# Optimization experiments

Measured on AMD Instinct MI355X. Metric: run time of the kernel, lower is better.

The kernel has to match this reference:

```python
import jax, jax.numpy as jnp
import numpy as np

B, S, D, H = 32, 578, 1024, 16  # seq = (384//16)**2 + 2 = 578
DH = D // H  # 64, per-head size
INIT_STD = 0.02


def setup_inputs() -> dict:
    key = jax.random.key(0)
    ks = jax.random.split(key, 7)
    hidden_states = jax.random.normal(ks[0], (B, S, D), dtype=jnp.float32)
    # Per-head Dense layers: stack H separate [D, DH] kernels -> [H, D, DH]
    Wq = jax.random.normal(ks[1], (H, D, DH), dtype=jnp.float32) * INIT_STD
    Wk = jax.random.normal(ks[2], (H, D, DH), dtype=jnp.float32) * INIT_STD
    Wv = jax.random.normal(ks[3], (H, D, DH), dtype=jnp.float32) * INIT_STD
    bq = jax.random.normal(ks[4], (H, DH), dtype=jnp.float32) * INIT_STD
    bk = jax.random.normal(ks[5], (H, DH), dtype=jnp.float32) * INIT_STD
    bv = jax.random.normal(ks[6], (H, DH), dtype=jnp.float32) * INIT_STD
    return {"hidden_states": hidden_states, "Wq": Wq, "bq": bq,
            "Wk": Wk, "bk": bk, "Wv": Wv, "bv": bv}


def reference(hidden_states, Wq, bq, Wk, bk, Wv, bv):
    # Per-head Dense projections (original: Python list of H Dense layers),
    # expressed as one batched einsum over the head axis.
    # hidden_states: [B, S, D]; W*: [H, D, E]; b*: [H, E]
    q = jnp.einsum('bsd,hde->bhse', hidden_states, Wq) + bq[None, :, None, :]
    k = jnp.einsum('bsd,hde->bhse', hidden_states, Wk) + bk[None, :, None, :]
    v = jnp.einsum('bsd,hde->bhse', hidden_states, Wv) + bv[None, :, None, :]
    scale = 1.0 / jnp.sqrt(jnp.asarray(DH, dtype=q.dtype))
    scores = jnp.einsum('bhse,bhte->bhst', q, k) * scale  # [B, H, S, S]
    probs = jax.nn.softmax(scores, axis=-1)  # stable_softmax; dropout p=0
    out = jnp.einsum('bhst,bhte->bhse', probs, v)  # [B, H, S, E]
    # concat heads along last axis -> [B, S, H*E]
    return out.transpose(0, 2, 1, 3).reshape(B, S, H * DH)
```

## Files before the change

kernel.cpp:

```cpp
#include <hip/hip_runtime.h>

typedef __attribute__((ext_vector_type(8))) short short8;
typedef __attribute__((ext_vector_type(4))) float f32x4;
typedef unsigned short u16;
typedef unsigned int u32;

#define B_ 32
#define S_ 578
#define D_ 1024
#define H_ 16
#define DH_ 64
#define M_ 18496
#define MP_ 18560
#define N_ 3072
#define K_ 1024
#define ST_ 640
#define BHROWS_ (B_ * H_ * S_ + 64)
#define SCALE2 0.18033688011112042f
#define CMAX 16.0f

__device__ __forceinline__ u16 f2bf(float x) {
  u32 u = __float_as_uint(x);
  u = (u + 0x7fffu + ((u >> 16) & 1u)) >> 16;
  return (u16)u;
}

__device__ __forceinline__ void gload_lds16(const u16* g, u16* l) {
  __builtin_amdgcn_global_load_lds((const __attribute__((address_space(1))) void*)g,
                                   (__attribute__((address_space(3))) void*)l, 16, 0, 0);
}

__global__ __launch_bounds__(256) void cvt_hidden(const float* __restrict__ in, u16* __restrict__ o) {
  long i = ((long)blockIdx.x * 256 + threadIdx.x) * 8;
  float4 f0 = *(const float4*)(in + i);
  float4 f1 = *(const float4*)(in + i + 4);
  short8 v;
  u16* p = (u16*)&v;
  p[0] = f2bf(f0.x); p[1] = f2bf(f0.y); p[2] = f2bf(f0.z); p[3] = f2bf(f0.w);
  p[4] = f2bf(f1.x); p[5] = f2bf(f1.y); p[6] = f2bf(f1.z); p[7] = f2bf(f1.w);
  *(short8*)(o + i) = v;
}

__global__ __launch_bounds__(256) void wt_kernel(const float* __restrict__ Wq, const float* __restrict__ Wk,
                                                 const float* __restrict__ Wv, u16* __restrict__ Wt) {
  const int d0 = blockIdx.x * 64;
  const int h = blockIdx.y;
  const int qkv = blockIdx.z;
  const float* W = (qkv == 0) ? Wq : ((qkv == 1) ? Wk : Wv);
  __shared__ float tile[64][65];
  const int t = threadIdx.x;
  {
    int e = t & 63, dr = t >> 6;
#pragma unroll
    for (int p = 0; p < 16; ++p) {
      int dd = dr + p * 4;
      tile[dd][e] = W[((long)h * D_ + d0 + dd) * DH_ + e];
    }
  }
  __syncthreads();
  {
    int dd = t & 63, er = t >> 6;
#pragma unroll
    for (int p = 0; p < 16; ++p) {
      int ee = er + p * 4;
      long n = (long)qkv * 1024 + h * 64 + ee;
      Wt[n * K_ + d0 + dd] = f2bf(tile[dd][ee]);
    }
  }
}

__global__ __launch_bounds__(256) void bias_kernel(const float* __restrict__ bq, const float* __restrict__ bk,
                                                   const float* __restrict__ bv, float* __restrict__ bias) {
  int i = blockIdx.x * 256 + threadIdx.x;
  if (i < 3072) {
    const float* src = (i < 1024) ? bq : ((i < 2048) ? bk : bv);
    bias[i] = src[i & 1023];
  }
}

__global__ __launch_bounds__(256) void qkv_gemm(const u16* __restrict__ A, const u16* __restrict__ Bt,
                                                const float* __restrict__ bias,
                                                u16* __restrict__ qb, u16* __restrict__ kb, u16* __restrict__ vbt) {
  __shared__ alignas(16) u16 As[128 * 32];
  __shared__ alignas(16) u16 Bs[128 * 32];
  const int tid = threadIdx.x, wave = tid >> 6, lane = tid & 63, quad = lane >> 4, l16 = lane & 15;
  const long m0 = (long)blockIdx.x * 128, n0 = (long)blockIdx.y * 128;
  const u16* Ag = A + m0 * K_;
  const u16* Bg = Bt + n0 * K_;

  f32x4 acc[4][4];
#pragma unroll
  for (int mi = 0; mi < 4; ++mi)
#pragma unroll
    for (int ni = 0; ni < 4; ++ni) { f32x4 z = {0.f, 0.f, 0.f, 0.f}; acc[mi][ni] = z; }

  const int srow = lane >> 2;
  const int gchunk = (lane & 3) ^ ((lane >> 3) & 3);
  const int scol = gchunk * 8;
  const int r0 = 32 * wave;
  const int sw = quad ^ ((l16 >> 1) & 3);
  const int rb = (wave >> 1) * 64 + l16;
  const int cb = (wave & 1) * 64 + l16;

  for (int it = 0; it < 32; ++it) {
    const int k0 = it * 32;
    gload_lds16(Ag + (long)(r0 + srow) * K_ + k0 + scol,      &As[r0 * 32 + lane * 8]);
    gload_lds16(Ag + (long)(r0 + 16 + srow) * K_ + k0 + scol, &As[(r0 + 16) * 32 + lane * 8]);
    gload_lds16(Bg + (long)(r0 + srow) * K_ + k0 + scol,      &Bs[r0 * 32 + lane * 8]);
    gload_lds16(Bg + (long)(r0 + 16 + srow) * K_ + k0 + scol, &Bs[(r0 + 16) * 32 + lane * 8]);
    __syncthreads();
    const short8* Asv = (const short8*)As;
    const short8* Bsv = (const short8*)Bs;
    short8 a[4], b2[4];
#pragma unroll
    for (int mi = 0; mi < 4; ++mi) a[mi] = Asv[(rb + mi * 16) * 4 + sw];
#pragma unroll
    for (int ni = 0; ni < 4; ++ni) b2[ni] = Bsv[(cb + ni * 16) * 4 + sw];
#pragma unroll
    for (int mi = 0; mi < 4; ++mi)
#pragma unroll
      for (int ni = 0; ni < 4; ++ni)
        acc[mi][ni] = __builtin_amdgcn_mfma_f32_16x16x32_bf16(a[mi], b2[ni], acc[mi][ni], 0, 0, 0);
    __syncthreads();
  }

  float bv4[4]; int hh[4], ee[4];
#pragma unroll
  for (int ni = 0; ni < 4; ++ni) {
    long n = n0 + (wave & 1) * 64 + ni * 16 + l16;
    bv4[ni] = bias[n];
    hh[ni] = (int)((n >> 6) & 15);
    ee[ni] = (int)(n & 63);
  }
  const int qkv = (int)(n0 >> 10);
  if (qkv == 2) {
#pragma unroll
    for (int mi = 0; mi < 4; ++mi) {
#pragma unroll
      for (int r = 0; r < 4; ++r) {
        long m = m0 + (wave >> 1) * 64 + mi * 16 + quad * 4 + r;
        if (m < M_) {
          unsigned bi = (unsigned)m / (unsigned)S_;
          unsigned si = (unsigned)m - bi * (unsigned)S_;
#pragma unroll
          for (int ni = 0; ni < 4; ++ni) {
            float v = acc[mi][ni][r] + bv4[ni];
            vbt[((long)(bi * H_ + hh[ni]) * DH_ + ee[ni]) * ST_ + si] = f2bf(v);
          }
        }
      }
    }
  } else {
    u16* dst = (qkv == 0) ? qb : kb;
#pragma unroll
    for (int mi = 0; mi < 4; ++mi) {
#pragma unroll
      for (int r = 0; r < 4; ++r) {
        long m = m0 + (wave >> 1) * 64 + mi * 16 + quad * 4 + r;
        if (m < M_) {
          unsigned bi = (unsigned)m / (unsigned)S_;
          unsigned si = (unsigned)m - bi * (unsigned)S_;
          long rowb = ((long)bi * H_) * S_ * DH_ + (long)si * DH_;
#pragma unroll
          for (int ni = 0; ni < 4; ++ni) {
            float v = acc[mi][ni][r] + bv4[ni];
            dst[rowb + (long)hh[ni] * (S_ * DH_) + ee[ni]] = f2bf(v);
          }
        }
      }
    }
  }
}

__global__ __launch_bounds__(256) void attn_kernel(const u16* __restrict__ qb, const u16* __restrict__ kb,
                                                   const u16* __restrict__ vbt, float* __restrict__ out) {
  __shared__ alignas(16) u16 Ks[64 * 64];
  __shared__ alignas(16) u16 Vs[64 * 64];
  __shared__ alignas(16) u16 Ps[4 * 16 * 72];
  const int tid = threadIdx.x, wave = tid >> 6, lane = tid & 63, quad = lane >> 4, l16 = lane & 15;
  const int qt = blockIdx.x, h = blockIdx.y, b = blockIdx.z;
  const long bh = (long)b * H_ + h;
  const u16* qp = qb + bh * S_ * DH_;
  const u16* kp = kb + bh * S_ * DH_;
  const u16* vtp = vbt + bh * DH_ * ST_;
  const int q0 = qt * 64;

  short8 qf0, qf1;
  {
    int row = q0 + wave * 16 + l16;
    const short8* qv = (const short8*)(qp + (long)row * DH_);
    qf0 = qv[quad];
    qf1 = qv[4 + quad];
  }

  f32x4 O[4];
#pragma unroll
  for (int et = 0; et < 4; ++et) { f32x4 z = {0.f, 0.f, 0.f, 0.f}; O[et] = z; }
  float lp[4] = {0.f, 0.f, 0.f, 0.f};

  const int srow0 = tid >> 3;
  const int slot = tid & 7;
  const int s0 = quad ^ (l16 & 7);

  for (int kt = 0; kt < 10; ++kt) {
    const int t0 = kt * 64;
    __syncthreads();
#pragma unroll
    for (int p = 0; p < 2; ++p) {
      int row = srow0 + 32 * p;
      int gch = slot ^ (row & 7);
      gload_lds16(kp + (long)(t0 + row) * DH_ + gch * 8, &Ks[(tid + 256 * p) * 8]);
      gload_lds16(vtp + (long)row * ST_ + t0 + gch * 8, &Vs[(tid + 256 * p) * 8]);
    }
    __syncthreads();

    float p[4][4];
    const short8* Kv8 = (const short8*)Ks;
#pragma unroll
    for (int jt = 0; jt < 4; ++jt) {
      f32x4 sacc = {0.f, 0.f, 0.f, 0.f};
      short8 kf0 = Kv8[(16 * jt + l16) * 8 + s0];
      short8 kf1 = Kv8[(16 * jt + l16) * 8 + ((quad + 4) ^ (l16 & 7))];
      sacc = __builtin_amdgcn_mfma_f32_16x16x32_bf16(qf0, kf0, sacc, 0, 0, 0);
      sacc = __builtin_amdgcn_mfma_f32_16x16x32_bf16(qf1, kf1, sacc, 0, 0, 0);
      bool valid = (t0 + 16 * jt + l16) < S_;
#pragma unroll
      for (int r = 0; r < 4; ++r) {
        float e = valid ? exp2f(sacc[r] * SCALE2 - CMAX) : 0.f;
        p[jt][r] = e;
        lp[r] += e;
      }
    }

    u16* Pw = Ps + wave * 16 * 72;
#pragma unroll
    for (int jt = 0; jt < 4; ++jt)
#pragma unroll
      for (int r = 0; r < 4; ++r)
        Pw[(quad * 4 + r) * 72 + 16 * jt + l16] = f2bf(p[jt][r]);

    const short8* Pv8 = (const short8*)(Ps + wave * 16 * 72);
    const short8* Vv8 = (const short8*)Vs;
#pragma unroll
    for (int ks = 0; ks < 2; ++ks) {
      short8 pa = Pv8[l16 * 9 + ks * 4 + quad];
#pragma unroll
      for (int et = 0; et < 4; ++et) {
        short8 vf = Vv8[(16 * et + l16) * 8 + ((ks * 4 + quad) ^ (l16 & 7))];
        O[et] = __builtin_amdgcn_mfma_f32_16x16x32_bf16(pa, vf, O[et], 0, 0, 0);
      }
    }
  }

  float inv[4];
#pragma unroll
  for (int r = 0; r < 4; ++r) {
    float s = lp[r];
    s += __shfl_xor(s, 1);
    s += __shfl_xor(s, 2);
    s += __shfl_xor(s, 4);
    s += __shfl_xor(s, 8);
    inv[r] = 1.0f / s;
  }
#pragma unroll
  for (int et = 0; et < 4; ++et)
#pragma unroll
    for (int r = 0; r < 4; ++r) {
      int s = q0 + wave * 16 + quad * 4 + r;
      if (s < S_) out[((long)b * S_ + s) * (H_ * DH_) + (long)h * DH_ + et * 16 + l16] = O[et][r] * inv[r];
    }
}

extern "C" void kernel_launch(void* const* d_in, const int* in_sizes, int n_in,
                              void* d_out, int out_size, void* d_ws, size_t ws_size,
                              hipStream_t stream) {
  const float* hs = (const float*)d_in[0];
  const float* Wq = (const float*)d_in[1];
  const float* bq = (const float*)d_in[2];
  const float* Wk = (const float*)d_in[3];
  const float* bk = (const float*)d_in[4];
  const float* Wv = (const float*)d_in[5];
  const float* bv = (const float*)d_in[6];
  float* out = (float*)d_out;

  u16* Abf = (u16*)d_ws;
  u16* Wt = Abf + (size_t)MP_ * K_;
  float* bias = (float*)(Wt + (size_t)N_ * K_);
  u16* qb = (u16*)(bias + N_);
  u16* kb = qb + (size_t)BHROWS_ * DH_;
  u16* vbt = kb + (size_t)BHROWS_ * DH_;

  cvt_hidden<<<dim3(9248), dim3(256), 0, stream>>>(hs, Abf);
  wt_kernel<<<dim3(16, 16, 3), dim3(256), 0, stream>>>(Wq, Wk, Wv, Wt);
  bias_kernel<<<dim3(12), dim3(256), 0, stream>>>(bq, bk, bv, bias);
  qkv_gemm<<<dim3(145, 24), dim3(256), 0, stream>>>(Abf, Wt, bias, qb, kb, vbt);
  attn_kernel<<<dim3(10, 16, 32), dim3(256), 0, stream>>>(qb, kb, vbt, out);
}
```

Measured before the change: 478.8 us.

## Deepen GEMM K-tile, remap GEMM blocks, and double per-wave query rows in attention

The QKV GEMM now loads 64-wide K tiles, which halves the number of barriers. It also uses a 1D grid whose block-index remap groups the N tiles sharing an M tile on neighbouring blocks, to improve L2 reuse of A. The attention kernel handles 128 queries per block (32 per wave), so each K/V tile loaded into LDS serves twice as many rows. S is now computed transposed (K as the A operand), the P stores are packed, and row sums are reduced through LDS. In exchange the kernel uses more registers and LDS, and the launch has fewer attention blocks, which lowers occupancy and parallelism.

```diff
diff --git a/kernel.cpp b/kernel.cpp
--- a/kernel.cpp
+++ b/kernel.cpp
@@ -81,10 +81,14 @@
 __global__ __launch_bounds__(256) void qkv_gemm(const u16* __restrict__ A, const u16* __restrict__ Bt,
                                                 const float* __restrict__ bias,
                                                 u16* __restrict__ qb, u16* __restrict__ kb, u16* __restrict__ vbt) {
-  __shared__ alignas(16) u16 As[128 * 32];
-  __shared__ alignas(16) u16 Bs[128 * 32];
+  __shared__ alignas(16) u16 As[128 * 64];
+  __shared__ alignas(16) u16 Bs[128 * 64];
   const int tid = threadIdx.x, wave = tid >> 6, lane = tid & 63, quad = lane >> 4, l16 = lane & 15;
-  const long m0 = (long)blockIdx.x * 128, n0 = (long)blockIdx.y * 128;
+  const int id = blockIdx.x;
+  const int jj = id >> 3;
+  const int m_t = jj / 3;
+  const int n_t = (id & 7) * 3 + (jj - m_t * 3);
+  const long m0 = (long)m_t * 128, n0 = (long)n_t * 128;
   const u16* Ag = A + m0 * K_;
   const u16* Bg = Bt + n0 * K_;
 
@@ -94,33 +98,36 @@
 #pragma unroll
     for (int ni = 0; ni < 4; ++ni) { f32x4 z = {0.f, 0.f, 0.f, 0.f}; acc[mi][ni] = z; }
 
-  const int srow = lane >> 2;
-  const int gchunk = (lane & 3) ^ ((lane >> 3) & 3);
-  const int scol = gchunk * 8;
-  const int r0 = 32 * wave;
-  const int sw = quad ^ ((l16 >> 1) & 3);
+  const int srow = tid >> 3;
+  const int gch8 = (((tid & 7) ^ ((tid >> 3) & 7))) * 8;
+  const int fsw = l16 & 7;
   const int rb = (wave >> 1) * 64 + l16;
   const int cb = (wave & 1) * 64 + l16;
 
-  for (int it = 0; it < 32; ++it) {
-    const int k0 = it * 32;
-    gload_lds16(Ag + (long)(r0 + srow) * K_ + k0 + scol,      &As[r0 * 32 + lane * 8]);
-    gload_lds16(Ag + (long)(r0 + 16 + srow) * K_ + k0 + scol, &As[(r0 + 16) * 32 + lane * 8]);
-    gload_lds16(Bg + (long)(r0 + srow) * K_ + k0 + scol,      &Bs[r0 * 32 + lane * 8]);
-    gload_lds16(Bg + (long)(r0 + 16 + srow) * K_ + k0 + scol, &Bs[(r0 + 16) * 32 + lane * 8]);
+  for (int it = 0; it < 16; ++it) {
+    const int k0 = it * 64;
+#pragma unroll
+    for (int i = 0; i < 4; ++i) {
+      gload_lds16(Ag + (long)(srow + 32 * i) * K_ + k0 + gch8, &As[(tid + 256 * i) * 8]);
+      gload_lds16(Bg + (long)(srow + 32 * i) * K_ + k0 + gch8, &Bs[(tid + 256 * i) * 8]);
+    }
     __syncthreads();
     const short8* Asv = (const short8*)As;
     const short8* Bsv = (const short8*)Bs;
-    short8 a[4], b2[4];
-#pragma unroll
-    for (int mi = 0; mi < 4; ++mi) a[mi] = Asv[(rb + mi * 16) * 4 + sw];
-#pragma unroll
-    for (int ni = 0; ni < 4; ++ni) b2[ni] = Bsv[(cb + ni * 16) * 4 + sw];
-#pragma unroll
-    for (int mi = 0; mi < 4; ++mi)
-#pragma unroll
-      for (int ni = 0; ni < 4; ++ni)
-        acc[mi][ni] = __builtin_amdgcn_mfma_f32_16x16x32_bf16(a[mi], b2[ni], acc[mi][ni], 0, 0, 0);
+#pragma unroll
+    for (int kk = 0; kk < 2; ++kk) {
+      short8 a[4], b2[4];
+      const int sl = (kk * 4 + quad) ^ fsw;
+#pragma unroll
+      for (int mi = 0; mi < 4; ++mi) a[mi] = Asv[(rb + mi * 16) * 8 + sl];
+#pragma unroll
+      for (int ni = 0; ni < 4; ++ni) b2[ni] = Bsv[(cb + ni * 16) * 8 + sl];
+#pragma unroll
+      for (int mi = 0; mi < 4; ++mi)
+#pragma unroll
+        for (int ni = 0; ni < 4; ++ni)
+          acc[mi][ni] = __builtin_amdgcn_mfma_f32_16x16x32_bf16(a[mi], b2[ni], acc[mi][ni], 0, 0, 0);
+    }
     __syncthreads();
   }
 
@@ -176,98 +183,120 @@
                                                    const u16* __restrict__ vbt, float* __restrict__ out) {
   __shared__ alignas(16) u16 Ks[64 * 64];
   __shared__ alignas(16) u16 Vs[64 * 64];
-  __shared__ alignas(16) u16 Ps[4 * 16 * 72];
+  __shared__ alignas(16) u16 Ps[4][32 * 72];
+  __shared__ float Ls[4][32];
   const int tid = threadIdx.x, wave = tid >> 6, lane = tid & 63, quad = lane >> 4, l16 = lane & 15;
   const int qt = blockIdx.x, h = blockIdx.y, b = blockIdx.z;
   const long bh = (long)b * H_ + h;
   const u16* qp = qb + bh * S_ * DH_;
   const u16* kp = kb + bh * S_ * DH_;
   const u16* vtp = vbt + bh * DH_ * ST_;
-  const int q0 = qt * 64;
-
-  short8 qf0, qf1;
-  {
-    int row = q0 + wave * 16 + l16;
+  const int q0 = qt * 128;
+
+  short8 qf[2][2];
+#pragma unroll
+  for (int g = 0; g < 2; ++g) {
+    int row = q0 + wave * 32 + g * 16 + l16;
     const short8* qv = (const short8*)(qp + (long)row * DH_);
-    qf0 = qv[quad];
-    qf1 = qv[4 + quad];
-  }
-
-  f32x4 O[4];
-#pragma unroll
-  for (int et = 0; et < 4; ++et) { f32x4 z = {0.f, 0.f, 0.f, 0.f}; O[et] = z; }
-  float lp[4] = {0.f, 0.f, 0.f, 0.f};
-
-  const int srow0 = tid >> 3;
-  const int slot = tid & 7;
-  const int s0 = quad ^ (l16 & 7);
+    qf[g][0] = qv[quad];
+    qf[g][1] = qv[4 + quad];
+  }
+
+  f32x4 O[2][4];
+#pragma unroll
+  for (int g = 0; g < 2; ++g)
+#pragma unroll
+    for (int et = 0; et < 4; ++et) { f32x4 z = {0.f, 0.f, 0.f, 0.f}; O[g][et] = z; }
+  float lp[2] = {0.f, 0.f};
+
+  const int srow = tid >> 3;
+  const int gch8 = (((tid & 7) ^ ((tid >> 3) & 7))) * 8;
+  const int fsw = l16 & 7;
 
   for (int kt = 0; kt < 10; ++kt) {
     const int t0 = kt * 64;
     __syncthreads();
 #pragma unroll
     for (int p = 0; p < 2; ++p) {
-      int row = srow0 + 32 * p;
-      int gch = slot ^ (row & 7);
-      gload_lds16(kp + (long)(t0 + row) * DH_ + gch * 8, &Ks[(tid + 256 * p) * 8]);
-      gload_lds16(vtp + (long)row * ST_ + t0 + gch * 8, &Vs[(tid + 256 * p) * 8]);
+      int row = srow + 32 * p;
+      gload_lds16(kp + (long)(t0 + row) * DH_ + gch8, &Ks[(tid + 256 * p) * 8]);
+      gload_lds16(vtp + (long)row * ST_ + t0 + gch8, &Vs[(tid + 256 * p) * 8]);
     }
     __syncthreads();
 
-    float p[4][4];
+    f32x4 sacc[4][2];
     const short8* Kv8 = (const short8*)Ks;
 #pragma unroll
     for (int jt = 0; jt < 4; ++jt) {
-      f32x4 sacc = {0.f, 0.f, 0.f, 0.f};
-      short8 kf0 = Kv8[(16 * jt + l16) * 8 + s0];
-      short8 kf1 = Kv8[(16 * jt + l16) * 8 + ((quad + 4) ^ (l16 & 7))];
-      sacc = __builtin_amdgcn_mfma_f32_16x16x32_bf16(qf0, kf0, sacc, 0, 0, 0);
-      sacc = __builtin_amdgcn_mfma_f32_16x16x32_bf16(qf1, kf1, sacc, 0, 0, 0);
-      bool valid = (t0 + 16 * jt + l16) < S_;
-#pragma unroll
-      for (int r = 0; r < 4; ++r) {
-        float e = valid ? exp2f(sacc[r] * SCALE2 - CMAX) : 0.f;
-        p[jt][r] = e;
-        lp[r] += e;
-      }
-    }
-
-    u16* Pw = Ps + wave * 16 * 72;
-#pragma unroll
-    for (int jt = 0; jt < 4; ++jt)
-#pragma unroll
-      for (int r = 0; r < 4; ++r)
-        Pw[(quad * 4 + r) * 72 + 16 * jt + l16] = f2bf(p[jt][r]);
-
-    const short8* Pv8 = (const short8*)(Ps + wave * 16 * 72);
+      short8 kf0 = Kv8[(jt * 16 + l16) * 8 + (quad ^ fsw)];
+      short8 kf1 = Kv8[(jt * 16 + l16) * 8 + ((4 + quad) ^ fsw)];
+#pragma unroll
+      for (int g = 0; g < 2; ++g) {
+        f32x4 z = {0.f, 0.f, 0.f, 0.f};
+        z = __builtin_amdgcn_mfma_f32_16x16x32_bf16(kf0, qf[g][0], z, 0, 0, 0);
+        z = __builtin_amdgcn_mfma_f32_16x16x32_bf16(kf1, qf[g][1], z, 0, 0, 0);
+        sacc[jt][g] = z;
+      }
+    }
+
+    u16* Pw = Ps[wave];
+#pragma unroll
+    for (int jt = 0; jt < 4; ++jt) {
+#pragma unroll
+      for (int g = 0; g < 2; ++g) {
+        float pv[4];
+#pragma unroll
+        for (int r = 0; r < 4; ++r) {
+          bool valid = (t0 + jt * 16 + quad * 4 + r) < S_;
+          float e = valid ? exp2f(sacc[jt][g][r] * SCALE2 - CMAX) : 0.f;
+          pv[r] = e;
+          lp[g] += e;
+        }
+        u32 lo = (u32)f2bf(pv[0]) | ((u32)f2bf(pv[1]) << 16);
+        u32 hi = (u32)f2bf(pv[2]) | ((u32)f2bf(pv[3]) << 16);
+        u32* dst = (u32*)(Pw + (g * 16 + l16) * 72 + jt * 16 + quad * 4);
+        dst[0] = lo;
+        dst[1] = hi;
+      }
+    }
+
+    const short8* Pv8 = (const short8*)Ps[wave];
     const short8* Vv8 = (const short8*)Vs;
 #pragma unroll
     for (int ks = 0; ks < 2; ++ks) {
-      short8 pa = Pv8[l16 * 9 + ks * 4 + quad];
-#pragma unroll
-      for (int et = 0; et < 4; ++et) {
-        short8 vf = Vv8[(16 * et + l16) * 8 + ((ks * 4 + quad) ^ (l16 & 7))];
-        O[et] = __builtin_amdgcn_mfma_f32_16x16x32_bf16(pa, vf, O[et], 0, 0, 0);
-      }
-    }
-  }
-
-  float inv[4];
-#pragma unroll
-  for (int r = 0; r < 4; ++r) {
-    float s = lp[r];
-    s += __shfl_xor(s, 1);
-    s += __shfl_xor(s, 2);
-    s += __shfl_xor(s, 4);
-    s += __shfl_xor(s, 8);
-    inv[r] = 1.0f / s;
-  }
-#pragma unroll
-  for (int et = 0; et < 4; ++et)
+      short8 vf[4];
+#pragma unroll
+      for (int et = 0; et < 4; ++et)
+        vf[et] = Vv8[(16 * et + l16) * 8 + ((ks * 4 + quad) ^ fsw)];
+#pragma unroll
+      for (int g = 0; g < 2; ++g) {
+        short8 pa = Pv8[(g * 16 + l16) * 9 + ks * 4 + quad];
+#pragma unroll
+        for (int et = 0; et < 4; ++et)
+          O[g][et] = __builtin_amdgcn_mfma_f32_16x16x32_bf16(pa, vf[et], O[g][et], 0, 0, 0);
+      }
+    }
+  }
+
+#pragma unroll
+  for (int g = 0; g < 2; ++g) {
+    float s = lp[g];
+    s += __shfl_xor(s, 16);
+    s += __shfl_xor(s, 32);
+    if (quad == 0) Ls[wave][g * 16 + l16] = 1.0f / s;
+  }
+  __builtin_amdgcn_s_waitcnt(0);
+#pragma unroll
+  for (int g = 0; g < 2; ++g)
 #pragma unroll
     for (int r = 0; r < 4; ++r) {
-      int s = q0 + wave * 16 + quad * 4 + r;
-      if (s < S_) out[((long)b * S_ + s) * (H_ * DH_) + (long)h * DH_ + et * 16 + l16] = O[et][r] * inv[r];
+      float invv = Ls[wave][g * 16 + quad * 4 + r];
+      int s = q0 + wave * 32 + g * 16 + quad * 4 + r;
+      if (s < S_) {
+#pragma unroll
+        for (int et = 0; et < 4; ++et)
+          out[((long)b * S_ + s) * (H_ * DH_) + (long)h * DH_ + et * 16 + l16] = O[g][et][r] * invv;
+      }
     }
 }
 
@@ -293,6 +322,6 @@
   cvt_hidden<<<dim3(9248), dim3(256), 0, stream>>>(hs, Abf);
   wt_kernel<<<dim3(16, 16, 3), dim3(256), 0, stream>>>(Wq, Wk, Wv, Wt);
   bias_kernel<<<dim3(12), dim3(256), 0, stream>>>(bq, bk, bv, bias);
-  qkv_gemm<<<dim3(145, 24), dim3(256), 0, stream>>>(Abf, Wt, bias, qb, kb, vbt);
-  attn_kernel<<<dim3(10, 16, 32), dim3(256), 0, stream>>>(qb, kb, vbt, out);
-}
+  qkv_gemm<<<dim3(3480), dim3(256), 0, stream>>>(Abf, Wt, bias, qb, kb, vbt);
+  attn_kernel<<<dim3(5, 16, 32), dim3(256), 0, stream>>>(qb, kb, vbt, out);
+}
```

Result: no change. 482.9 us (+0.9%).
